# Kernel tuning notes

Hardware: AMD Instinct MI355X
Metric: run time of the kernel (lower is better)

## Reference

```python
import jax, jax.numpy as jnp
import numpy as np

B, M = 2, 8192          # clouds per batch, points per cloud (N = B*M)
K_NEAR, K_FAR, K_SMOOTH = 8, 16, 8
T_LOC, T_CON = 0.1, 0.5
EPS = 1e-8


def setup_inputs() -> dict:
    key = jax.random.key(0)
    k1, k2 = jax.random.split(key)
    scores = jax.random.uniform(k1, (B * M,), dtype=jnp.float32)          # in [0,1]
    coords = jax.random.normal(k2, (B * M, 3), dtype=jnp.float32) * 2.0   # point positions
    batch_ids = (jnp.arange(B * M, dtype=jnp.int32) // M).astype(jnp.int32)
    return {"scores": scores, "coords": coords, "batch_ids": batch_ids}


def _knn_global(coords):
    """Per-cloud brute-force kNN (self included as first neighbor, like pointops.knn_query).
    coords: (N,3) -> global indices (N, K_FAR)."""
    c = coords.reshape(B, M, 3)

    def per_cloud(cb):  # cb: (M,3)
        sq = jnp.sum(cb * cb, axis=-1)                      # (M,)
        d2 = sq[:, None] + sq[None, :] - 2.0 * (cb @ cb.T)  # (M,M) squared dists
        _, idx = jax.lax.top_k(-d2, K_FAR)                  # (M,K_FAR) smallest dists
        return idx

    idx = jax.vmap(per_cloud)(c)                            # (B,M,K_FAR) local indices
    idx = idx + (jnp.arange(B, dtype=idx.dtype) * M)[:, None, None]
    return idx.reshape(B * M, K_FAR)


def _loss_terms(scores, coords, idx):
    # --- locality: neighbors (incl. self) should have similar scores ---
    nb = idx[:, :K_NEAR]                                    # (N,k)
    score_diff = jnp.abs(scores[:, None] - scores[nb])      # (N,k)
    dists = jnp.linalg.norm(coords[:, None, :] - coords[nb], axis=2)  # (N,k)
    w = jnp.exp(-dists / T_LOC)
    loss_loc = jnp.sum(w * score_diff ** 2) / jnp.clip(jnp.sum(w), 1e-8)

    # --- contrastive: near similar, far dissimilar ---
    sim_pos = 1.0 - jnp.abs(scores[:, None] - scores[idx[:, :K_NEAR]])
    sim_neg = 1.0 - jnp.abs(scores[:, None] - scores[idx[:, K_NEAR:K_FAR]])
    loss_pos = -jnp.mean(jnp.log(jax.nn.sigmoid(sim_pos / T_CON) + EPS))
    loss_neg = -jnp.mean(jnp.log(1.0 - jax.nn.sigmoid(sim_neg / T_CON) + EPS))
    loss_con = loss_pos + loss_neg

    # --- distribution: sorted scores match uniform linspace per cloud ---
    sb = jnp.sort(scores.reshape(B, M), axis=1)             # (B,M)
    target = jnp.linspace(0.0, 1.0, M, dtype=scores.dtype)  # (M,)
    loss_dist = jnp.mean(jnp.mean((sb - target[None, :]) ** 2, axis=1))

    # --- smoothness: score close to neighbor mean ---
    nmean = jnp.mean(scores[idx[:, :K_SMOOTH]], axis=1)     # (N,)
    loss_smooth = jnp.mean((scores - nmean) ** 2)

    return loss_loc, loss_con, loss_dist, loss_smooth


def reference(scores, coords, batch_ids):
    del batch_ids  # equal-sized clouds; batch structure is (B, M) by construction
    idx = _knn_global(coords)
    l_loc, l_con, l_dist, l_smooth = _loss_terms(scores, coords, idx)
    total = 1.0 * l_loc + 0.5 * l_con + 0.3 * l_dist + 0.2 * l_smooth
    return total
```

## Files before the change

### kernel.cpp

```cpp
#include <hip/hip_runtime.h>
#include <hip/hip_bf16.h>
#include <math.h>

#define BB 2
#define MM 8192
#define NN (BB * MM)
#define NBATCH (NN / 16)
#define NCELL 4096
#define LOSS_BLOCKS 1024

#define PART_OFF   0
#define RANK_OFF   24576
#define IDX_OFF    90112
#define PK_OFF     1138688
#define SS_OFF     1400832
#define CELLID_OFF 1466368
#define CUR_OFF    1531904
#define BBLO_OFF   1564672
#define BBHI_OFF   1581056

__device__ __forceinline__ unsigned fenc(float f) {
    unsigned u = __float_as_uint(f);
    return (u & 0x80000000u) ? ~u : (u | 0x80000000u);
}
__device__ __forceinline__ float fdec(unsigned u) {
    return __uint_as_float((u & 0x80000000u) ? (u & 0x7FFFFFFFu) : ~u);
}

__device__ __forceinline__ unsigned mort3(unsigned x, unsigned y, unsigned z) {
    unsigned m = 0;
#pragma unroll
    for (int i = 0; i < 4; ++i) {
        m |= ((x >> i) & 1u) << (3 * i);
        m |= ((y >> i) & 1u) << (3 * i + 1);
        m |= ((z >> i) & 1u) << (3 * i + 2);
    }
    return m;
}

__global__ __launch_bounds__(1024) void countscan_kernel(const float* __restrict__ coords,
                                                         int* __restrict__ cellid,
                                                         int* __restrict__ cursor,
                                                         unsigned* __restrict__ bblo,
                                                         unsigned* __restrict__ bbhi) {
    __shared__ int scnt[2 * NCELL];
    __shared__ int wsum[16];
    const int tid = threadIdx.x, lane = tid & 63, wv = tid >> 6;
#pragma unroll
    for (int j = 0; j < 8; ++j) scnt[tid + 1024 * j] = 0;
    __syncthreads();
#pragma unroll
    for (int j = 0; j < 16; ++j) {
        const int i = tid + 1024 * j;
        float x = coords[3 * i], y = coords[3 * i + 1], z = coords[3 * i + 2];
        int cx = min(15, max(0, (int)floorf(x) + 8));
        int cy = min(15, max(0, (int)floorf(y) + 8));
        int cz = min(15, max(0, (int)floorf(z) + 8));
        int cid = (i >> 13) * NCELL + (int)mort3((unsigned)cx, (unsigned)cy, (unsigned)cz);
        cellid[i] = cid;
        atomicAdd(&scnt[cid], 1);
    }
    __syncthreads();
    int v[8]; int run = 0;
#pragma unroll
    for (int i = 0; i < 8; ++i) { int t = scnt[tid * 8 + i]; v[i] = run; run += t; }
    int inc = run;
#pragma unroll
    for (int off = 1; off < 64; off <<= 1) {
        int y = __shfl_up(inc, off);
        if (lane >= off) inc += y;
    }
    int laneExcl = inc - run;
    if (lane == 63) wsum[wv] = inc;
    __syncthreads();
    int wbase = 0;
#pragma unroll
    for (int w = 0; w < 16; ++w) wbase += (w < wv) ? wsum[w] : 0;
    const int base = wbase + laneExcl;
#pragma unroll
    for (int i = 0; i < 8; ++i) cursor[tid * 8 + i] = base + v[i];
#pragma unroll
    for (int j = 0; j < 4; ++j) {
        bblo[tid * 4 + j] = 0xFFFFFFFFu;
        bbhi[tid * 4 + j] = 0u;
    }
}

__global__ void scatter_kernel(const float* __restrict__ coords, const float* __restrict__ scores,
                               const int* __restrict__ cellid, int* __restrict__ cursor,
                               float4* __restrict__ pk_s, float* __restrict__ s_s,
                               unsigned* __restrict__ bblo, unsigned* __restrict__ bbhi) {
    int i = blockIdx.x * 256 + threadIdx.x;
    if (i < NN) {
        int pos = atomicAdd(&cursor[cellid[i]], 1);
        float x = coords[3 * i], y = coords[3 * i + 1], z = coords[3 * i + 2];
        float sq = fmaf(x, x, fmaf(y, y, z * z));
        pk_s[pos] = make_float4(x, y, z, sq);
        s_s[pos] = scores[i];
        const int b4 = (pos >> 4) * 4;
        atomicMin(&bblo[b4 + 0], fenc(x));
        atomicMin(&bblo[b4 + 1], fenc(y));
        atomicMin(&bblo[b4 + 2], fenc(z));
        atomicMax(&bbhi[b4 + 0], fenc(x));
        atomicMax(&bbhi[b4 + 1], fenc(y));
        atomicMax(&bbhi[b4 + 2], fenc(z));
    }
}

__device__ __forceinline__ void sort16(unsigned (&a)[16]) {
#pragma unroll
    for (int p2 = 1; p2 < 16; p2 <<= 1) {
#pragma unroll
        for (int k2 = p2; k2 >= 1; k2 >>= 1) {
#pragma unroll
            for (int j2 = k2 % p2; j2 + k2 < 16; j2 += 2 * k2) {
#pragma unroll
                for (int i2 = 0; i2 < k2; ++i2) {
                    if (i2 + j2 + k2 < 16) {
                        if (((i2 + j2) / (2 * p2)) == ((i2 + j2 + k2) / (2 * p2))) {
                            unsigned x = a[i2 + j2], y = a[i2 + j2 + k2];
                            a[i2 + j2]      = min(x, y);
                            a[i2 + j2 + k2] = max(x, y);
                        }
                    }
                }
            }
        }
    }
}

__device__ __forceinline__ void truncmerge(unsigned (&slot)[16], const unsigned (&kb)[16]) {
    unsigned m[16];
#pragma unroll
    for (int k = 0; k < 16; ++k) m[k] = min(slot[k], kb[15 - k]);
#pragma unroll
    for (int st = 8; st >= 1; st >>= 1) {
#pragma unroll
        for (int i = 0; i < 16; ++i) {
            if ((i & st) == 0) {
                unsigned lo = min(m[i], m[i + st]);
                unsigned hi = max(m[i], m[i + st]);
                m[i] = lo; m[i + st] = hi;
            }
        }
    }
#pragma unroll
    for (int k = 0; k < 16; ++k) slot[k] = m[k];
}

__global__ __launch_bounds__(1024) void knn_kernel(const float4* __restrict__ pk_s,
                                                   const float* __restrict__ s_s,
                                                   const unsigned* __restrict__ bblo,
                                                   const unsigned* __restrict__ bbhi,
                                                   int* __restrict__ out_idx,
                                                   int* __restrict__ out_rank) {
    __shared__ unsigned lds_k[16][16][64];
    __shared__ int lds_i[16][64];
    const int tid = threadIdx.x, lane = tid & 63;
    const int wv = __builtin_amdgcn_readfirstlane(tid >> 6);
    const int qbase = blockIdx.x * 64;
    const int cloudbase = (qbase >> 13) << 13;
    const float4 p = pk_s[qbase + lane];
    const int sb0 = (qbase - cloudbase) >> 4;
    const int r = sb0 & 15;
    const int ownb = (wv >= r && wv < r + 4) ? (sb0 + (wv - r)) : -1;
    const float4* __restrict__ pc = pk_s + cloudbase;
    const int bbase = cloudbase >> 4;

    unsigned slot[16];
#pragma unroll
    for (int k = 0; k < 16; ++k) slot[k] = 0x7F000000u + (unsigned)k;
    float t_f = 3.0e38f;

    auto batchU = [&](int bi) {
        unsigned kb[16];
#pragma unroll
        for (int i = 0; i < 16; ++i) {
            const int j = bi * 16 + i;
            const float4 c = pc[j];
            float dot = fmaf(p.x, c.x, fmaf(p.y, c.y, p.z * c.z));
            float d2  = fmaf(-2.0f, dot, p.w + c.w);
            kb[i] = (__float_as_uint(d2) & 0xFFFFE000u) | (unsigned)j;
        }
        sort16(kb);
        truncmerge(slot, kb);
        t_f = fminf(t_f, __uint_as_float((slot[15] & 0xFFFFE000u) + 0x2000u));
    };

    if (ownb >= 0) batchU(ownb);
#pragma unroll
    for (int k = 0; k < 16; ++k) lds_k[wv][k][lane] = slot[k];
    __syncthreads();
    unsigned mg[16];
#pragma unroll
    for (int k = 0; k < 16; ++k) mg[k] = lds_k[r][k][lane];
#pragma unroll
    for (int w2 = 1; w2 < 4; ++w2) {
        unsigned ob[16];
#pragma unroll
        for (int k = 0; k < 16; ++k) ob[k] = lds_k[r + w2][k][lane];
        truncmerge(mg, ob);
    }
    __syncthreads();
    if (wv == r) {
#pragma unroll
        for (int k = 0; k < 16; ++k) slot[k] = mg[k];
    } else {
#pragma unroll
        for (int k = 0; k < 16; ++k) slot[k] = 0x7F000000u + (unsigned)k;
    }
    t_f = __uint_as_float((mg[15] & 0xFFFFE000u) + 0x2000u);

    const uint4* __restrict__ blo4 = (const uint4*)bblo;
    const uint4* __restrict__ bhi4 = (const uint4*)bbhi;
    uint4 lo = blo4[bbase + wv];
    uint4 hi = bhi4[bbase + wv];
    for (int k2 = 0; k2 < 32; ++k2) {
        const int bi = wv + (k2 << 4);
        uint4 lo_n, hi_n;
        if (k2 + 1 < 32) {
            lo_n = blo4[bbase + bi + 16];
            hi_n = bhi4[bbase + bi + 16];
        }
        if (bi != ownb) {
            float dx = fmaxf(fmaxf(fdec(lo.x) - p.x, p.x - fdec(hi.x)), 0.f);
            float dy = fmaxf(fmaxf(fdec(lo.y) - p.y, p.y - fdec(hi.y)), 0.f);
            float dz = fmaxf(fmaxf(fdec(lo.z) - p.z, p.z - fdec(hi.z)), 0.f);
            float lb = fmaf(dx, dx, fmaf(dy, dy, dz * dz));
            if (__any(fmaf(lb, 0.999f, -1e-5f) < t_f)) batchU(bi);
        }
        lo = lo_n; hi = hi_n;
    }

#pragma unroll
    for (int k = 0; k < 16; ++k) lds_k[wv][k][lane] = slot[k];

    for (int half = 8; half >= 1; half >>= 1) {
        __syncthreads();
        if (wv < half) {
            unsigned a[16], m[16];
#pragma unroll
            for (int k = 0; k < 16; ++k) a[k] = lds_k[wv][k][lane];
#pragma unroll
            for (int k = 0; k < 16; ++k) m[k] = min(a[k], lds_k[wv + half][15 - k][lane]);
#pragma unroll
            for (int st = 8; st >= 1; st >>= 1) {
#pragma unroll
                for (int i = 0; i < 16; ++i) {
                    if ((i & st) == 0) {
                        unsigned lo2 = min(m[i], m[i + st]);
                        unsigned hi2 = max(m[i], m[i + st]);
                        m[i] = lo2; m[i + st] = hi2;
                    }
                }
            }
#pragma unroll
            for (int k = 0; k < 16; ++k) lds_k[wv][k][lane] = m[k];
        }
    }
    __syncthreads();
    if (wv == 0) {
#pragma unroll
        for (int k = 0; k < 16; ++k)
            out_idx[(qbase + lane) * 16 + k] = (int)(lds_k[0][k][lane] & 0x1FFFu) + cloudbase;
    }

    {
        const float s = s_s[qbase + lane];
        const float* __restrict__ sc = s_s + cloudbase;
        int rank = 0;
        const int j0 = wv * 512;
        for (int jj = 0; jj < 512; jj += 16) {
#pragma unroll
            for (int i = 0; i < 16; ++i) {
                rank += (sc[j0 + jj + i] < s) ? 1 : 0;
            }
        }
        lds_i[wv][lane] = rank;
        __syncthreads();
        if (wv == 0) {
            int rsum = 0;
#pragma unroll
            for (int w = 0; w < 16; ++w) rsum += lds_i[w][lane];
            out_rank[qbase + lane] = rsum;
        }
    }
}

__global__ __launch_bounds__(256) void loss_kernel(const float* __restrict__ s_s,
                                                   const float4* __restrict__ pk_s,
                                                   const int* __restrict__ knn,
                                                   const int* __restrict__ rank,
                                                   float* __restrict__ partial) {
    __shared__ float red[4][6];
    const int t = blockIdx.x * 256 + threadIdx.x;
    const int q = t >> 4, k = t & 15;
    const int nb = knn[t];
    const float s  = s_s[q];
    const float sn = s_s[nb];
    const float diff = fabsf(s - sn);
    const float sim = 1.0f - diff;
    const float sg = 1.0f / (1.0f + expf(-2.0f * sim));

    float a_wd = 0.f, a_w = 0.f, a_pos = 0.f, a_neg = 0.f, snk = 0.f;
    if (k < 8) {
        float4 pq = pk_s[q];
        float4 pn = pk_s[nb];
        float dx = pq.x - pn.x, dy = pq.y - pn.y, dz = pq.z - pn.z;
        float d = sqrtf(dx * dx + dy * dy + dz * dz);
        float w = expf(-10.0f * d);
        a_wd = w * diff * diff;
        a_w  = w;
        a_pos = logf(sg + 1e-8f);
        snk = sn;
    } else {
        a_neg = logf(1.0f - sg + 1e-8f);
    }

    float nsum = snk;
#pragma unroll
    for (int off = 1; off < 16; off <<= 1) nsum += __shfl_xor(nsum, off);

    float a_sm = 0.f, a_di = 0.f;
    if (k == 0) {
        float t1 = s - nsum * 0.125f;
        a_sm = t1 * t1;
        float t2 = s - (float)rank[q] * (1.0f / 8191.0f);
        a_di = t2 * t2;
    }

#pragma unroll
    for (int off = 1; off < 64; off <<= 1) {
        a_wd  += __shfl_xor(a_wd, off);
        a_w   += __shfl_xor(a_w, off);
        a_pos += __shfl_xor(a_pos, off);
        a_neg += __shfl_xor(a_neg, off);
        a_sm  += __shfl_xor(a_sm, off);
        a_di  += __shfl_xor(a_di, off);
    }
    const int wv = threadIdx.x >> 6;
    if ((threadIdx.x & 63) == 0) {
        red[wv][0] = a_wd; red[wv][1] = a_w; red[wv][2] = a_pos;
        red[wv][3] = a_neg; red[wv][4] = a_sm; red[wv][5] = a_di;
    }
    __syncthreads();
    if (threadIdx.x < 6) {
        float v = red[0][threadIdx.x] + red[1][threadIdx.x] +
                  red[2][threadIdx.x] + red[3][threadIdx.x];
        partial[threadIdx.x * LOSS_BLOCKS + blockIdx.x] = v;
    }
}

__global__ __launch_bounds__(1024) void fin_kernel(const float* __restrict__ partial,
                                                   float* __restrict__ out) {
    __shared__ float red[16][6];
    const int tid = threadIdx.x;
    float a[6];
#pragma unroll
    for (int term = 0; term < 6; ++term) a[term] = partial[term * LOSS_BLOCKS + tid];
#pragma unroll
    for (int off = 1; off < 64; off <<= 1) {
#pragma unroll
        for (int term = 0; term < 6; ++term) a[term] += __shfl_xor(a[term], off);
    }
    if ((tid & 63) == 0) {
#pragma unroll
        for (int term = 0; term < 6; ++term) red[tid >> 6][term] = a[term];
    }
    __syncthreads();
    if (tid == 0) {
        float acc[6];
#pragma unroll
        for (int term = 0; term < 6; ++term) {
            float v = 0.f;
#pragma unroll
            for (int w = 0; w < 16; ++w) v += red[w][term];
            acc[term] = v;
        }
        float l_loc = acc[0] / fmaxf(acc[1], 1e-8f);
        float l_pos = -acc[2] / (float)(NN * 8);
        float l_neg = -acc[3] / (float)(NN * 8);
        float l_sm  = acc[4] / (float)NN;
        float l_di  = acc[5] / (float)NN;
        out[0] = l_loc + 0.5f * (l_pos + l_neg) + 0.3f * l_di + 0.2f * l_sm;
    }
}

extern "C" void kernel_launch(void* const* d_in, const int* in_sizes, int n_in,
                              void* d_out, int out_size, void* d_ws, size_t ws_size,
                              hipStream_t stream) {
    const float* scores = (const float*)d_in[0];
    const float* coords = (const float*)d_in[1];
    (void)in_sizes; (void)n_in; (void)out_size; (void)ws_size;

    char* ws = (char*)d_ws;
    float*    part  = (float*)(ws + PART_OFF);
    int*      rank  = (int*)(ws + RANK_OFF);
    int*      knn   = (int*)(ws + IDX_OFF);
    float4*   pk_s  = (float4*)(ws + PK_OFF);
    float*    s_s   = (float*)(ws + SS_OFF);
    int*      cellid= (int*)(ws + CELLID_OFF);
    int*      cursor= (int*)(ws + CUR_OFF);
    unsigned* bblo  = (unsigned*)(ws + BBLO_OFF);
    unsigned* bbhi  = (unsigned*)(ws + BBHI_OFF);
    float*    out   = (float*)d_out;

    countscan_kernel<<<1, 1024, 0, stream>>>(coords, cellid, cursor, bblo, bbhi);
    scatter_kernel<<<64, 256, 0, stream>>>(coords, scores, cellid, cursor, pk_s, s_s, bblo, bbhi);
    knn_kernel<<<256, 1024, 0, stream>>>(pk_s, s_s, bblo, bbhi, knn, rank);
    loss_kernel<<<LOSS_BLOCKS, 256, 0, stream>>>(s_s, pk_s, knn, rank, part);
    fin_kernel<<<1, 1024, 0, stream>>>(part, out);
}
```

Measured before the change: 150.2 us.

## Split kNN candidate scan across two blocks per query group and merge later

The kNN kernel is split so each 64-query group is handled by two blocks, each scanning half of the cloud's candidate batches. The partial top-16 lists go to workspace and are merged by a new rankmerge kernel, which also takes over the rank counting. batchU also gains an early check that skips the sort and merge when no lane's batch minimum beats its current 16th-best. This doubles the grid to fill more CUs, at the cost of an extra kernel launch, duplicated seed work, and a global round trip for the partial results.

```diff
diff --git a/kernel.cpp b/kernel.cpp
--- a/kernel.cpp
+++ b/kernel.cpp
@@ -8,16 +8,17 @@
 #define NBATCH (NN / 16)
 #define NCELL 4096
 #define LOSS_BLOCKS 1024
+#define PARTK_HALF 262144
 
 #define PART_OFF   0
 #define RANK_OFF   24576
 #define IDX_OFF    90112
-#define PK_OFF     1138688
-#define SS_OFF     1400832
-#define CELLID_OFF 1466368
-#define CUR_OFF    1531904
-#define BBLO_OFF   1564672
-#define BBHI_OFF   1581056
+#define PK_OFF     2187264
+#define SS_OFF     2449408
+#define CELLID_OFF 2514944
+#define CUR_OFF    2580480
+#define BBLO_OFF   2613248
+#define BBHI_OFF   2629632
 
 __device__ __forceinline__ unsigned fenc(float f) {
     unsigned u = __float_as_uint(f);
@@ -148,22 +149,23 @@
     for (int k = 0; k < 16; ++k) slot[k] = m[k];
 }
 
-__global__ __launch_bounds__(1024) void knn_kernel(const float4* __restrict__ pk_s,
-                                                   const float* __restrict__ s_s,
-                                                   const unsigned* __restrict__ bblo,
-                                                   const unsigned* __restrict__ bbhi,
-                                                   int* __restrict__ out_idx,
-                                                   int* __restrict__ out_rank) {
+__global__ __launch_bounds__(1024) void knn_part_kernel(const float4* __restrict__ pk_s,
+                                                        const unsigned* __restrict__ bblo,
+                                                        const unsigned* __restrict__ bbhi,
+                                                        unsigned* __restrict__ partk) {
     __shared__ unsigned lds_k[16][16][64];
-    __shared__ int lds_i[16][64];
     const int tid = threadIdx.x, lane = tid & 63;
     const int wv = __builtin_amdgcn_readfirstlane(tid >> 6);
-    const int qbase = blockIdx.x * 64;
+    const int qb = blockIdx.x >> 1;
+    const int h  = blockIdx.x & 1;
+    const int qbase = qb * 64;
     const int cloudbase = (qbase >> 13) << 13;
     const float4 p = pk_s[qbase + lane];
     const int sb0 = (qbase - cloudbase) >> 4;
     const int r = sb0 & 15;
-    const int ownb = (wv >= r && wv < r + 4) ? (sb0 + (wv - r)) : -1;
+    const bool owner = (h == (sb0 >> 8));
+    const int seedb = (wv >= r && wv < r + 4) ? (sb0 + (wv - r)) : -1;
+    const int ownb = owner ? seedb : -1;
     const float4* __restrict__ pc = pk_s + cloudbase;
     const int bbase = cloudbase >> 4;
 
@@ -172,7 +174,7 @@
     for (int k = 0; k < 16; ++k) slot[k] = 0x7F000000u + (unsigned)k;
     float t_f = 3.0e38f;
 
-    auto batchU = [&](int bi) {
+    auto batchU = [&](int bi, bool force) {
         unsigned kb[16];
 #pragma unroll
         for (int i = 0; i < 16; ++i) {
@@ -182,12 +184,17 @@
             float d2  = fmaf(-2.0f, dot, p.w + c.w);
             kb[i] = (__float_as_uint(d2) & 0xFFFFE000u) | (unsigned)j;
         }
-        sort16(kb);
-        truncmerge(slot, kb);
-        t_f = fminf(t_f, __uint_as_float((slot[15] & 0xFFFFE000u) + 0x2000u));
+        unsigned kmin = kb[0];
+#pragma unroll
+        for (int i = 1; i < 16; ++i) kmin = min(kmin, kb[i]);
+        if (force || __any(kmin < slot[15])) {
+            sort16(kb);
+            truncmerge(slot, kb);
+            t_f = fminf(t_f, __uint_as_float((slot[15] & 0xFFFFE000u) + 0x2000u));
+        }
     };
 
-    if (ownb >= 0) batchU(ownb);
+    if (seedb >= 0) batchU(seedb, true);
 #pragma unroll
     for (int k = 0; k < 16; ++k) lds_k[wv][k][lane] = slot[k];
     __syncthreads();
@@ -202,7 +209,7 @@
         truncmerge(mg, ob);
     }
     __syncthreads();
-    if (wv == r) {
+    if (owner && wv == r) {
 #pragma unroll
         for (int k = 0; k < 16; ++k) slot[k] = mg[k];
     } else {
@@ -213,12 +220,13 @@
 
     const uint4* __restrict__ blo4 = (const uint4*)bblo;
     const uint4* __restrict__ bhi4 = (const uint4*)bbhi;
-    uint4 lo = blo4[bbase + wv];
-    uint4 hi = bhi4[bbase + wv];
-    for (int k2 = 0; k2 < 32; ++k2) {
-        const int bi = wv + (k2 << 4);
+    const int hbase = h * 256;
+    uint4 lo = blo4[bbase + hbase + wv];
+    uint4 hi = bhi4[bbase + hbase + wv];
+    for (int k2 = 0; k2 < 16; ++k2) {
+        const int bi = hbase + wv + (k2 << 4);
         uint4 lo_n, hi_n;
-        if (k2 + 1 < 32) {
+        if (k2 + 1 < 16) {
             lo_n = blo4[bbase + bi + 16];
             hi_n = bhi4[bbase + bi + 16];
         }
@@ -227,7 +235,7 @@
             float dy = fmaxf(fmaxf(fdec(lo.y) - p.y, p.y - fdec(hi.y)), 0.f);
             float dz = fmaxf(fmaxf(fdec(lo.z) - p.z, p.z - fdec(hi.z)), 0.f);
             float lb = fmaf(dx, dx, fmaf(dy, dy, dz * dz));
-            if (__any(fmaf(lb, 0.999f, -1e-5f) < t_f)) batchU(bi);
+            if (__any(fmaf(lb, 0.999f, -1e-5f) < t_f)) batchU(bi, false);
         }
         lo = lo_n; hi = hi_n;
     }
@@ -262,28 +270,47 @@
     if (wv == 0) {
 #pragma unroll
         for (int k = 0; k < 16; ++k)
-            out_idx[(qbase + lane) * 16 + k] = (int)(lds_k[0][k][lane] & 0x1FFFu) + cloudbase;
-    }
-
-    {
-        const float s = s_s[qbase + lane];
-        const float* __restrict__ sc = s_s + cloudbase;
-        int rank = 0;
-        const int j0 = wv * 512;
-        for (int jj = 0; jj < 512; jj += 16) {
-#pragma unroll
-            for (int i = 0; i < 16; ++i) {
-                rank += (sc[j0 + jj + i] < s) ? 1 : 0;
-            }
-        }
-        lds_i[wv][lane] = rank;
-        __syncthreads();
-        if (wv == 0) {
-            int rsum = 0;
-#pragma unroll
-            for (int w = 0; w < 16; ++w) rsum += lds_i[w][lane];
-            out_rank[qbase + lane] = rsum;
-        }
+            partk[h * PARTK_HALF + qb * 1024 + k * 64 + lane] = lds_k[0][k][lane];
+    }
+}
+
+__global__ __launch_bounds__(1024) void rankmerge_kernel(const float* __restrict__ s_s,
+                                                         unsigned* __restrict__ partk,
+                                                         int* __restrict__ out_rank) {
+    __shared__ int lds_i[16][64];
+    const int tid = threadIdx.x, lane = tid & 63;
+    const int wv = __builtin_amdgcn_readfirstlane(tid >> 6);
+    const int qbase = blockIdx.x * 64;
+    const int cloudbase = (qbase >> 13) << 13;
+    const float s = s_s[qbase + lane];
+    const float* __restrict__ sc = s_s + cloudbase;
+    int rank = 0;
+    const int j0 = wv * 512;
+    for (int jj = 0; jj < 512; jj += 16) {
+#pragma unroll
+        for (int i = 0; i < 16; ++i) {
+            rank += (sc[j0 + jj + i] < s) ? 1 : 0;
+        }
+    }
+    lds_i[wv][lane] = rank;
+    __syncthreads();
+    if (wv == 0) {
+        int rsum = 0;
+#pragma unroll
+        for (int w = 0; w < 16; ++w) rsum += lds_i[w][lane];
+        out_rank[qbase + lane] = rsum;
+
+        unsigned a[16], b[16];
+#pragma unroll
+        for (int k = 0; k < 16; ++k) a[k] = partk[blockIdx.x * 1024 + k * 64 + lane];
+#pragma unroll
+        for (int k = 0; k < 16; ++k) b[k] = partk[PARTK_HALF + blockIdx.x * 1024 + k * 64 + lane];
+        __asm__ __volatile__("s_waitcnt vmcnt(0)" ::: "memory");
+        truncmerge(a, b);
+        int* out_idx = (int*)partk;
+#pragma unroll
+        for (int k = 0; k < 16; ++k)
+            out_idx[(qbase + lane) * 16 + k] = (int)(a[k] & 0x1FFFu) + cloudbase;
     }
 }
 
@@ -396,6 +423,7 @@
     char* ws = (char*)d_ws;
     float*    part  = (float*)(ws + PART_OFF);
     int*      rank  = (int*)(ws + RANK_OFF);
+    unsigned* partk = (unsigned*)(ws + IDX_OFF);
     int*      knn   = (int*)(ws + IDX_OFF);
     float4*   pk_s  = (float4*)(ws + PK_OFF);
     float*    s_s   = (float*)(ws + SS_OFF);
@@ -407,7 +435,8 @@
 
     countscan_kernel<<<1, 1024, 0, stream>>>(coords, cellid, cursor, bblo, bbhi);
     scatter_kernel<<<64, 256, 0, stream>>>(coords, scores, cellid, cursor, pk_s, s_s, bblo, bbhi);
-    knn_kernel<<<256, 1024, 0, stream>>>(pk_s, s_s, bblo, bbhi, knn, rank);
+    knn_part_kernel<<<512, 1024, 0, stream>>>(pk_s, bblo, bbhi, partk);
+    rankmerge_kernel<<<256, 1024, 0, stream>>>(s_s, partk, rank);
     loss_kernel<<<LOSS_BLOCKS, 256, 0, stream>>>(s_s, pk_s, knn, rank, part);
     fin_kernel<<<1, 1024, 0, stream>>>(part, out);
 }
```

New measurement: 164.9 us. 9.8% more time.
